# Kernel optimization log

Measured on AMD Instinct MI355X. Metric: run time of the kernel, lower is better.

## Reference

```python
import math
import jax, jax.numpy as jnp
import numpy as np

K = 16
EPS = 1e-05
EPS_VAR = 1e-04


def _gelu(x):
    # tanh-approx GELU, identical to the torch module's _gelu
    c = math.sqrt(2.0 / math.pi)
    return 0.5 * x * (1.0 + jnp.tanh(c * (x + 0.044715 * x ** 3)))


def setup_inputs() -> dict:
    key = jax.random.key(0)
    k1, k2, k3, k4 = jax.random.split(key, 4)
    B, T, D = 4, 4096, 4096
    x = jax.random.normal(k1, (B, T, D), dtype=jnp.float32)
    ema_mean = 0.1 * jax.random.normal(k2, (D,), dtype=jnp.float32)
    # ensure variance is positive and realistic
    ema_sq = ema_mean ** 2 + jax.random.uniform(k3, (D,), dtype=jnp.float32, minval=0.5, maxval=1.5)
    ema_out = jax.random.normal(k4, (D,), dtype=jnp.float32)
    return {
        "x": x,
        "ema_mean": ema_mean,
        "ema_sq": ema_sq,
        "ema_out": ema_out,
        "log_tau": jnp.asarray(math.log(2.0), dtype=jnp.float32),
        "log_beta_up": jnp.asarray(math.log(math.exp(0.5) - 1.0), dtype=jnp.float32),
        "log_gamma": jnp.asarray(math.log(math.exp(1.0) - 1.0), dtype=jnp.float32),
        "logit_beta_fam": jnp.asarray(-1.386, dtype=jnp.float32),
    }


def reference(x, ema_mean, ema_sq, ema_out, log_tau, log_beta_up, log_gamma, logit_beta_fam):
    sg = jax.lax.stop_gradient
    B, T, D = x.shape
    k = min(K, D // 2)

    # scalar params (tau is only used inside torch.no_grad -> stop-grad)
    tau = sg(jnp.exp(log_tau))
    beta_up = jax.nn.softplus(log_beta_up)
    gamma = jax.nn.softplus(log_gamma)
    beta_fam = jax.nn.sigmoid(logit_beta_fam)

    out = _gelu(x)  # [B,T,D], differentiable path

    # ----- no_grad z-score + top/bot-k index selection -----
    mu = sg(ema_mean)
    var = jnp.maximum(sg(ema_sq) - mu ** 2, EPS_VAR)
    std = jnp.sqrt(var)
    z = (sg(x) - mu) / (std + EPS)          # [B,T,D], detached
    abs_z = jnp.abs(z)
    _, topk_idx = jax.lax.top_k(abs_z, k)   # [B,T,k] largest |z|
    _, botk_idx = jax.lax.top_k(-abs_z, k)  # [B,T,k] smallest |z|

    # ----- gate construction (gather + scatter along D) -----
    z_topk = jnp.take_along_axis(z, topk_idx, axis=-1)            # [B,T,k]
    g_topk = jnp.clip(1.0 + beta_up * jnp.tanh(gamma * z_topk), 0.1, 8.0)

    N = B * T
    rows = jnp.arange(N)[:, None]                                  # [N,1]
    gate = jnp.ones((N, D), dtype=x.dtype)
    gate = gate.at[rows, topk_idx.reshape(N, k)].set(g_topk.reshape(N, k))
    gate = gate.at[rows, botk_idx.reshape(N, k)].set(
        jnp.broadcast_to(beta_fam.astype(x.dtype), (N, k)))
    gate = gate.reshape(B, T, D)

    # ----- cosine-similarity gate (all no_grad) -----
    out_d = sg(out)
    out_n = out_d / jnp.maximum(jnp.linalg.norm(out_d, axis=-1, keepdims=True), 1e-12)
    eo = sg(ema_out)
    ema_n = eo / jnp.maximum(jnp.linalg.norm(eo), 1e-12)           # [D]
    cos_sim = jnp.clip(jnp.sum(out_n * ema_n, axis=-1), -1.0, 1.0)  # [B,T]
    gate_cos = jnp.exp(-tau * cos_sim)[..., None]                   # [B,T,1]

    return out * gate * gate_cos
```

## Files before the change

### kernel.cpp

```cpp
#include <hip/hip_runtime.h>
#include <stdint.h>

#define TPB   256
#define D_DIM 4096
#define EPW   16
#define NVEC  (EPW/4)
#define CAP   256
#define NQ    (CAP/64)
#define KSEL  16
#define THI0  2.5f
#define TLO0  0.02f

#define WS_STDP 0
#define WS_MI   D_DIM
#define WS_SCAL (2*D_DIM)
#define WS_GC   8200
#define WS_REC_F 24584

typedef float vfloat4 __attribute__((ext_vector_type(4)));

__device__ __forceinline__ float fast_rcp(float v)  { return __builtin_amdgcn_rcpf(v); }
__device__ __forceinline__ float fast_exp2(float v) { return __builtin_amdgcn_exp2f(v); }

#define GELU_AN (-2.30220819f)
#define GELU_BN (-0.10294331f)
#define TWO_LOG2E (2.8853900817779268f)
#define LOG2E     (1.4426950408889634f)

__device__ __forceinline__ float gelu_fast(float x) {
    float x2 = x * x;
    float s  = fmaf(x2, GELU_BN, GELU_AN);
    float nq = x * s;
    float ex = fast_exp2(nq);
    return x * fast_rcp(1.0f + ex);
}

__device__ __forceinline__ float tanh_fast_pm(float y2l) {
    float ex = fast_exp2(y2l);
    float r  = fast_rcp(1.0f + ex);
    return fmaf(-2.0f, r, 1.0f);
}

__device__ __forceinline__ float top_gate(float zz, float beta_up, float kg) {
    float g = fmaf(beta_up, tanh_fast_pm(zz * kg), 1.0f);
    return fminf(fmaxf(g, 0.1f), 8.0f);
}

__device__ __forceinline__ unsigned long long make_key_top(float zp, unsigned int d) {
    const unsigned int zb = __float_as_uint(zp);
    const unsigned int pb = zb & 0x7fffffffu;
    const unsigned int klo = 0xFFFFE000u | ((~d & 0xFFFu) << 1) | (zb >> 31);
    return ((unsigned long long)pb << 32) | klo;
}
__device__ __forceinline__ unsigned long long make_key_bot(float zp, unsigned int d) {
    const unsigned int zb = __float_as_uint(zp);
    const unsigned int pb = (zb & 0x7fffffffu) ^ 0x7fffffffu;
    const unsigned int klo = 0xFFFFE000u | ((~d & 0xFFFu) << 1) | (zb >> 31);
    return ((unsigned long long)pb << 32) | klo;
}

__device__ __forceinline__ unsigned int bf16_hi(float v) {
    unsigned int u = __float_as_uint(v);
    u = (u + 0x7FFFu + ((u >> 16) & 1u)) >> 16;
    return u & 0xFFFFu;
}

__global__ __launch_bounds__(256) void precomp(
    const float* __restrict__ em, const float* __restrict__ eq,
    const float* __restrict__ eo,
    const float* __restrict__ lt, const float* __restrict__ lb,
    const float* __restrict__ lg, const float* __restrict__ lf,
    float* __restrict__ ws)
{
    __shared__ float red[4];
    const int tid = threadIdx.x;
    unsigned int* wsu = (unsigned int*)ws;
    float e2 = 0.0f;
    for (int i = 0; i < D_DIM / 256; ++i) {
        const int d = i * 256 + tid;
        const float mu  = em[d];
        const float mu2 = __fmul_rn(mu, mu);
        float var = __fsub_rn(eq[d], mu2);
        var = fmaxf(var, 1e-4f);
        const float stdp = __fadd_rn(sqrtf(var), 1e-5f);
        ws[WS_STDP + d] = stdp;
        const float invv = 1.0f / stdp;
        wsu[WS_MI + d] = (bf16_hi(mu) << 16) | bf16_hi(invv);
        const float e = eo[d];
        e2 = fmaf(e, e, e2);
    }
    #pragma unroll
    for (int off = 32; off; off >>= 1) e2 += __shfl_xor(e2, off);
    if ((tid & 63) == 0) red[tid >> 6] = e2;
    __syncthreads();
    if (tid == 0) {
        const float t  = red[0] + red[1] + red[2] + red[3];
        const float en = sqrtf(t);
        ws[WS_SCAL + 0] = expf(lt[0]);
        ws[WS_SCAL + 1] = log1pf(expf(lb[0]));
        ws[WS_SCAL + 2] = log1pf(expf(lg[0]));
        ws[WS_SCAL + 3] = 1.0f / (1.0f + expf(-lf[0]));
        ws[WS_SCAL + 4] = 1.0f / fmaxf(en, 1e-12f);
    }
}

__global__ __launch_bounds__(TPB, 4) void fused_gelu_gate(
    const float* __restrict__ x,
    const float* __restrict__ ema_mean,
    const float* __restrict__ ema_out,
    float* __restrict__ ws,
    unsigned long long* __restrict__ recs,
    float* __restrict__ out)
{
    __shared__ unsigned long long lists[2 * CAP];
    __shared__ float red[4][2];
    __shared__ unsigned int cnt[2];
    const int tid = threadIdx.x;
    const int ln  = tid & 63;
    const int wv  = tid >> 6;
    const long long base = (long long)blockIdx.x * D_DIM;

    if (tid < 2) cnt[tid] = 0u;
    __syncthreads();

    const float tau      = ws[WS_SCAL + 0];
    const float beta_up  = ws[WS_SCAL + 1];
    const float kg       = ws[WS_SCAL + 2] * TWO_LOG2E;
    const float beta_fam = ws[WS_SCAL + 3];
    const float inv_en   = ws[WS_SCAL + 4];
    const unsigned int* mip = (const unsigned int*)ws + WS_MI;

    float o_r[EPW];
    float s_o2 = 0.0f, s_dot = 0.0f;
    unsigned int maskT = 0u, maskB = 0u;

    #pragma unroll
    for (int i = 0; i < NVEC; ++i) {
        const int off = (i * TPB + tid) * 4;
        const float4 xv = *(const float4*)(x + base + off);
        const uint4  mv = *(const uint4*)(mip + off);
        const float4 ev = *(const float4*)(ema_out + off);
        const float xs[4] = {xv.x, xv.y, xv.z, xv.w};
        const unsigned int mis[4] = {mv.x, mv.y, mv.z, mv.w};
        const float es[4] = {ev.x, ev.y, ev.z, ev.w};
        #pragma unroll
        for (int j = 0; j < 4; ++j) {
            const int e = i * 4 + j;
            const float xx = xs[j];
            const float mu = __uint_as_float(mis[j] & 0xFFFF0000u);
            const float iv = __uint_as_float(mis[j] << 16);
            const float zz = (xx - mu) * iv;
            const float og = gelu_fast(xx);
            o_r[e] = og;
            s_o2  = fmaf(og, og, s_o2);
            s_dot = fmaf(og, es[j], s_dot);
            const float az = fabsf(zz);
            maskT |= (az >= THI0) ? (1u << e) : 0u;
            maskB |= (az <= TLO0) ? (1u << e) : 0u;
        }
    }

    {
        unsigned int mT = maskT;
        while (mT) {
            const int e = __ffs(mT) - 1; mT &= mT - 1u;
            const unsigned int d = (unsigned int)(((e >> 2) * TPB + tid) * 4 + (e & 3));
            const float xx   = x[base + d];
            const float mu   = ema_mean[d];
            const float stdp = ws[WS_STDP + d];
            const float zp   = __fdiv_rn(__fsub_rn(xx, mu), stdp);
            const unsigned int p = atomicAdd(&cnt[0], 1u);
            if (p < CAP) lists[p] = make_key_top(zp, d);
        }
        unsigned int mB = maskB;
        while (mB) {
            const int e = __ffs(mB) - 1; mB &= mB - 1u;
            const unsigned int d = (unsigned int)(((e >> 2) * TPB + tid) * 4 + (e & 3));
            const float xx   = x[base + d];
            const float mu   = ema_mean[d];
            const float stdp = ws[WS_STDP + d];
            const float zp   = __fdiv_rn(__fsub_rn(xx, mu), stdp);
            const unsigned int p = atomicAdd(&cnt[1], 1u);
            if (p < CAP) lists[CAP + p] = make_key_bot(zp, d);
        }
    }

    #pragma unroll
    for (int off = 32; off; off >>= 1) {
        s_o2  += __shfl_xor(s_o2, off);
        s_dot += __shfl_xor(s_dot, off);
    }
    if (ln == 0) { red[wv][0] = s_o2; red[wv][1] = s_dot; }
    __syncthreads();

    float t_o2 = 0.0f, t_dot = 0.0f;
    #pragma unroll
    for (int w = 0; w < TPB / 64; ++w) { t_o2 += red[w][0]; t_dot += red[w][1]; }

    {
        unsigned int cT = cnt[0], cB = cnt[1];
        float thi = THI0, tlo = TLO0;
        int tries = 0;
        while ((cT < (unsigned)KSEL || cT > (unsigned)CAP ||
                cB < (unsigned)KSEL || cB > (unsigned)CAP) && tries < 20) {
            if (cT < (unsigned)KSEL) thi *= 0.5f; else if (cT > (unsigned)CAP) thi *= 1.5f;
            if (cB < (unsigned)KSEL) tlo *= 2.0f; else if (cB > (unsigned)CAP) tlo *= 0.6666f;
            __syncthreads();
            if (tid < 2) cnt[tid] = 0u;
            __syncthreads();
            for (int e = 0; e < EPW; ++e) {
                const unsigned int d = (unsigned int)(((e >> 2) * TPB + tid) * 4 + (e & 3));
                const float xx   = x[base + d];
                const float mu   = ema_mean[d];
                const float stdp = ws[WS_STDP + d];
                const float zp   = __fdiv_rn(__fsub_rn(xx, mu), stdp);
                const float az   = fabsf(zp);
                if (az >= thi) {
                    const unsigned int p = atomicAdd(&cnt[0], 1u);
                    if (p < CAP) lists[p] = make_key_top(zp, d);
                } else if (az <= tlo) {
                    const unsigned int p = atomicAdd(&cnt[1], 1u);
                    if (p < CAP) lists[CAP + p] = make_key_bot(zp, d);
                }
            }
            __syncthreads();
            cT = cnt[0]; cB = cnt[1];
            ++tries;
        }
    }

    const float on = sqrtf(t_o2);
    float cs = (t_dot * inv_en) / fmaxf(on, 1e-12f);
    cs = fminf(fmaxf(cs, -1.0f), 1.0f);
    const float gc = fast_exp2(-tau * cs * LOG2E);
    if (tid == 0) ws[WS_GC + blockIdx.x] = gc;

    #pragma unroll
    for (int i = 0; i < NVEC; ++i) {
        const int off = (i * TPB + tid) * 4;
        vfloat4 ov;
        ov.x = o_r[i * 4 + 0] * gc;
        ov.y = o_r[i * 4 + 1] * gc;
        ov.z = o_r[i * 4 + 2] * gc;
        ov.w = o_r[i * 4 + 3] * gc;
        __builtin_nontemporal_store(ov, (vfloat4*)(out + base + off));
    }

    if (wv >= 2) return;
    {
        const int ph = wv;
        unsigned int m = cnt[ph];
        if (m > CAP) m = CAP;
        unsigned long long key[NQ];
        #pragma unroll
        for (int q = 0; q < NQ; ++q) {
            const unsigned int p = (unsigned int)ln + ((unsigned int)q << 6);
            key[q] = (p < m) ? lists[ph * CAP + p] : 0ull;
        }
        unsigned long long* rr = recs + (long long)blockIdx.x * 32 + ph * KSEL;
        #pragma unroll 1
        for (int it = 0; it < KSEL; ++it) {
            unsigned long long k = 0ull;
            #pragma unroll
            for (int q = 0; q < NQ; ++q) k = (key[q] > k) ? key[q] : k;
            #pragma unroll
            for (int off = 32; off; off >>= 1) {
                const unsigned long long o = __shfl_xor(k, off);
                if (o > k) k = o;
            }
            if (ln == 0) {
                unsigned long long rec;
                if (k == 0ull) {
                    rec = ((unsigned long long)__float_as_uint(1.0f) << 32) | 0xFFFFu;
                } else {
                    const unsigned int klo = (unsigned int)(k & 0xffffffffu);
                    const unsigned int d   = (~(klo >> 1)) & 0xFFFu;
                    float g;
                    if (ph == 0) {
                        const unsigned int pb = (unsigned int)(k >> 32);
                        const float azf = __uint_as_float(pb);
                        const float zw  = (klo & 1u) ? -azf : azf;
                        g = top_gate(zw, beta_up, kg);
                    } else {
                        g = beta_fam;
                    }
                    rec = ((unsigned long long)__float_as_uint(g) << 32) | d;
                }
                rr[it] = rec;
            }
            #pragma unroll
            for (int q = 0; q < NQ; ++q) if (key[q] == k) key[q] = 0ull;
        }
    }
}

__global__ __launch_bounds__(256) void fixup(
    const float* __restrict__ x,
    const float* __restrict__ ws,
    const unsigned long long* __restrict__ recs,
    float* __restrict__ out)
{
    const int gid = blockIdx.x * 256 + threadIdx.x;
    const unsigned long long rec = recs[gid];
    const unsigned int d = (unsigned int)(rec & 0xFFFFu);
    if (d < (unsigned)D_DIM) {
        const int row = gid >> 5;
        const float gc = ws[WS_GC + row];
        const float g  = __uint_as_float((unsigned int)(rec >> 32));
        const long long idx = (long long)row * D_DIM + d;
        out[idx] = gelu_fast(x[idx]) * g * gc;
    }
}

extern "C" void kernel_launch(void* const* d_in, const int* in_sizes, int n_in,
                              void* d_out, int out_size, void* d_ws, size_t ws_size,
                              hipStream_t stream) {
    const float* x  = (const float*)d_in[0];
    const float* em = (const float*)d_in[1];
    const float* eq = (const float*)d_in[2];
    const float* eo = (const float*)d_in[3];
    const float* lt = (const float*)d_in[4];
    const float* lb = (const float*)d_in[5];
    const float* lg = (const float*)d_in[6];
    const float* lf = (const float*)d_in[7];
    float* o  = (float*)d_out;
    float* ws = (float*)d_ws;
    unsigned long long* recs = (unsigned long long*)(ws + WS_REC_F);
    const int rows = in_sizes[0] / D_DIM;
    precomp<<<dim3(1), dim3(256), 0, stream>>>(em, eq, eo, lt, lb, lg, lf, ws);
    fused_gelu_gate<<<dim3(rows), dim3(TPB), 0, stream>>>(x, em, eo, ws, recs, o);
    fixup<<<dim3(rows * 32 / 256), dim3(256), 0, stream>>>(x, ws, recs, o);
}
```

Before: 203.0 us.

## Replace serial top-k wave reduction with parallel rank-based selection

Replaces the 16-round wave-level max-and-remove selection of the top and bottom candidates with a rank computation. Each of the 256 threads compares one candidate against all others in its list and writes it straight to its rank slot. Candidate capacity is halved to 128 and launch bounds ask for 8 blocks per CU to raise occupancy. The aims are to drop the serialized shuffle loop and idle waves at the kernel tail, and to cut LDS use. In exchange it risks candidate overflow with the smaller cap. It also no longer writes sentinel records when fewer than 16 candidates exist.

After: 323.9 us. 1.6x slower.

```diff
diff --git a/kernel.cpp b/kernel.cpp
--- a/kernel.cpp
+++ b/kernel.cpp
@@ -5,8 +5,7 @@
 #define D_DIM 4096
 #define EPW   16
 #define NVEC  (EPW/4)
-#define CAP   256
-#define NQ    (CAP/64)
+#define CAP   128
 #define KSEL  16
 #define THI0  2.5f
 #define TLO0  0.02f
@@ -104,7 +103,7 @@
     }
 }
 
-__global__ __launch_bounds__(TPB, 4) void fused_gelu_gate(
+__global__ __launch_bounds__(TPB, 8) void fused_gelu_gate(
     const float* __restrict__ x,
     const float* __restrict__ ema_mean,
     const float* __restrict__ ema_out,
@@ -246,50 +245,33 @@
         __builtin_nontemporal_store(ov, (vfloat4*)(out + base + off));
     }
 
-    if (wv >= 2) return;
     {
-        const int ph = wv;
-        unsigned int m = cnt[ph];
-        if (m > CAP) m = CAP;
-        unsigned long long key[NQ];
-        #pragma unroll
-        for (int q = 0; q < NQ; ++q) {
-            const unsigned int p = (unsigned int)ln + ((unsigned int)q << 6);
-            key[q] = (p < m) ? lists[ph * CAP + p] : 0ull;
-        }
-        unsigned long long* rr = recs + (long long)blockIdx.x * 32 + ph * KSEL;
-        #pragma unroll 1
-        for (int it = 0; it < KSEL; ++it) {
-            unsigned long long k = 0ull;
-            #pragma unroll
-            for (int q = 0; q < NQ; ++q) k = (key[q] > k) ? key[q] : k;
-            #pragma unroll
-            for (int off = 32; off; off >>= 1) {
-                const unsigned long long o = __shfl_xor(k, off);
-                if (o > k) k = o;
+        const unsigned int cT = min(cnt[0], (unsigned)CAP);
+        const unsigned int cB = min(cnt[1], (unsigned)CAP);
+        const int half = tid >> 7;
+        const unsigned int i = (unsigned int)(tid & 127);
+        const unsigned int m = half ? cB : cT;
+        if (i < m) {
+            const unsigned long long* lp = &lists[half * CAP];
+            const unsigned long long k_i = lp[i];
+            unsigned int rank = 0;
+            for (unsigned int j = 0; j < m; ++j)
+                rank += (lp[j] > k_i) ? 1u : 0u;
+            if (rank < (unsigned)KSEL) {
+                const unsigned int klo = (unsigned int)(k_i & 0xffffffffu);
+                const unsigned int d   = (~(klo >> 1)) & 0xFFFu;
+                float g;
+                if (half == 0) {
+                    const unsigned int pb = (unsigned int)(k_i >> 32);
+                    const float azf = __uint_as_float(pb);
+                    const float zw  = (klo & 1u) ? -azf : azf;
+                    g = top_gate(zw, beta_up, kg);
+                } else {
+                    g = beta_fam;
+                }
+                recs[(long long)blockIdx.x * 32 + half * KSEL + rank] =
+                    ((unsigned long long)__float_as_uint(g) << 32) | d;
             }
-            if (ln == 0) {
-                unsigned long long rec;
-                if (k == 0ull) {
-                    rec = ((unsigned long long)__float_as_uint(1.0f) << 32) | 0xFFFFu;
-                } else {
-                    const unsigned int klo = (unsigned int)(k & 0xffffffffu);
-                    const unsigned int d   = (~(klo >> 1)) & 0xFFFu;
-                    float g;
-                    if (ph == 0) {
-                        const unsigned int pb = (unsigned int)(k >> 32);
-                        const float azf = __uint_as_float(pb);
-                        const float zw  = (klo & 1u) ? -azf : azf;
-                        g = top_gate(zw, beta_up, kg);
-                    } else {
-                        g = beta_fam;
-                    }
-                    rec = ((unsigned long long)__float_as_uint(g) << 32) | d;
-                }
-                rr[it] = rec;
-            }
-            #pragma unroll
-            for (int q = 0; q < NQ; ++q) if (key[q] == k) key[q] = 0ull;
         }
     }
 }
```
